# Kernel optimization log

Measured on AMD Instinct MI355X. Metric: run time of the kernel, lower is better.

## Reference

```python
import jax, jax.numpy as jnp
import numpy as np

B, S, D, W, P = 32, 512, 768, 256, 1024


def setup_inputs() -> dict:
    key = jax.random.key(0)
    k_h, k_len, k_pair, k_w1, k_w2 = jax.random.split(key, 5)
    h = jax.random.normal(k_h, (B, S, D), dtype=jnp.float32)
    # ragged word spans: each word covers 1 or 2 contiguous subwords; total <= S
    word_len = jax.random.randint(k_len, (B, W), 1, 3, dtype=jnp.int32)  # in {1,2}
    word_start = jnp.concatenate(
        [jnp.zeros((B, 1), jnp.int32), jnp.cumsum(word_len, axis=1)[:, :-1]], axis=1
    )
    # word-index pairs per configuration; -1 means "use zero embedding"
    pair_idx = jax.random.randint(k_pair, (B, P, 2), 0, W + 1, dtype=jnp.int32) - 1
    w1 = jax.random.normal(k_w1, (2 * D, 300), dtype=jnp.float32) * 0.02
    b1 = jnp.zeros((300,), jnp.float32)
    w2 = jax.random.normal(k_w2, (300, 4), dtype=jnp.float32) * 0.02
    b2 = jnp.zeros((4,), jnp.float32)
    return {"h": h, "w1": w1, "b1": b1, "w2": w2, "b2": b2,
            "word_start": word_start, "word_len": word_len, "pair_idx": pair_idx}


def reference(h, w1, b1, w2, b2, word_start, word_len, pair_idx):
    # --- mean-pool subword embeddings per word via prefix sums (segment mean) ---
    csum = jnp.cumsum(h, axis=1)                                   # [B,S,D]
    csum = jnp.concatenate([jnp.zeros_like(csum[:, :1]), csum], 1)  # [B,S+1,D]
    end = word_start + word_len                                     # [B,W]
    seg_sum = (jnp.take_along_axis(csum, end[:, :, None], axis=1)
               - jnp.take_along_axis(csum, word_start[:, :, None], axis=1))
    word_emb = seg_sum / word_len[:, :, None].astype(h.dtype)       # [B,W,D]
    # --- per-pair gather with -1 -> zero vector ---
    valid = (pair_idx >= 0)                                         # [B,P,2]
    idx = jnp.maximum(pair_idx, 0).reshape(h.shape[0], -1)          # [B,2P]
    emb = jnp.take_along_axis(word_emb, idx[:, :, None], axis=1)    # [B,2P,D]
    emb = emb.reshape(pair_idx.shape[0], pair_idx.shape[1], 2, -1)
    emb = jnp.where(valid[..., None], emb, jnp.zeros((), h.dtype))
    mlp_input = emb.reshape(-1, 2 * h.shape[-1])                    # [B*P, 2D]
    # --- tiny MLP + softmax (dropout is identity in eval) ---
    x = jnp.tanh(mlp_input @ w1 + b1)
    return jax.nn.softmax(x @ w2 + b2, axis=-1)                     # [B*P, 4]
```

## Files before the change

### kernel.cpp

```cpp
#include <hip/hip_runtime.h>
#include <cstddef>
#include <cstdint>

#define Bb   32
#define Ss   512
#define Dd   768
#define Ww   256
#define Pp   1024
#define NH   300
#define SLOT1 320
#define NPAD 640
#define Mm   (Bb * Ww)

typedef __attribute__((ext_vector_type(8))) short bf16x8;
typedef __attribute__((ext_vector_type(4))) float f32x4;

#define GPTR(p) ((const __attribute__((address_space(1))) void*)(p))
#define LPTR(p) ((__attribute__((address_space(3))) void*)(p))

__device__ __forceinline__ unsigned short f2bf(float x) {
    unsigned u = __builtin_bit_cast(unsigned, x);
    u += 0x7fffu + ((u >> 16) & 1u);
    return (unsigned short)(u >> 16);
}
__device__ __forceinline__ float bf2f(unsigned short u) {
    return __builtin_bit_cast(float, (unsigned)u << 16);
}
__device__ __forceinline__ float fast_tanh(float x) {
    x = fminf(fmaxf(x, -15.0f), 15.0f);
    float e = __expf(2.0f * x);
    return 1.0f - 2.0f * __builtin_amdgcn_rcpf(e + 1.0f);
}

__global__ __launch_bounds__(192) void prep_kernel(
    const float* __restrict__ h, const float* __restrict__ w1,
    const int* __restrict__ word_start, const int* __restrict__ word_len,
    unsigned short* __restrict__ emb, unsigned short* __restrict__ bmatT,
    unsigned short* __restrict__ zrow)
{
    const int bid = blockIdx.x;
    const int t   = threadIdx.x;
    if (bid < Mm) {
        const int m   = bid;
        const int b   = m >> 8;
        const int s0  = word_start[m];
        const int len = word_len[m];
        const float* p = h + (size_t)b * (Ss * Dd) + (size_t)s0 * Dd + t * 4;
        float4 v = *(const float4*)p;
        if (len == 2) {
            float4 v2 = *(const float4*)(p + Dd);
            v.x = (v.x + v2.x) * 0.5f;
            v.y = (v.y + v2.y) * 0.5f;
            v.z = (v.z + v2.z) * 0.5f;
            v.w = (v.w + v2.w) * 0.5f;
        }
        ushort4 o = make_ushort4(f2bf(v.x), f2bf(v.y), f2bf(v.z), f2bf(v.w));
        *(ushort4*)(emb + (size_t)m * Dd + t * 4) = o;
    } else if (bid < Mm + 4 * NPAD) {
        const int rb = bid - Mm;
        const int n  = rb >> 2;
        const int k  = ((rb & 3) * 192) + t;
        float v = 0.0f;
        if (n < NH)                          v = w1[(size_t)k * NH + n];
        else if (n >= SLOT1 && n < SLOT1+NH) v = w1[(size_t)(Dd + k) * NH + (n - SLOT1)];
        bmatT[(size_t)n * Dd + k] = f2bf(v);
    } else {
        if (t < NPAD / 4)
            *(ushort4*)(zrow + t * 4) = make_ushort4(0, 0, 0, 0);
    }
}

__global__ __launch_bounds__(256) void gemm_kernel(
    const unsigned short* __restrict__ emb, const unsigned short* __restrict__ bmatT,
    unsigned short* __restrict__ proj)
{
    __shared__ bf16x8 Al[2][4][128];
    __shared__ bf16x8 Bl[2][4][128];

    const int bid = blockIdx.x;
    const int t   = threadIdx.x;

    const int swz   = (bid & 7) * 40 + (bid >> 3);
    const int mBase = (swz / 5) * 128;
    const int nBase = (swz % 5) * 128;

    const int srow = t & 127;
    const int skb  = t >> 7;
    const unsigned short* srcA = emb   + (size_t)(mBase + srow) * Dd + (skb << 3);
    const unsigned short* srcB = bmatT + (size_t)(nBase + srow) * Dd + (skb << 3);
    char* ldsA = (char*)&Al[0][0][0] + t * 16;
    char* ldsB = (char*)&Bl[0][0][0] + t * 16;

    const int lane = t & 63;
    const int w    = t >> 6;
    const int wr   = w >> 1;
    const int wc   = w & 1;
    const int fr   = lane & 15;
    const int kb   = lane >> 4;

    f32x4 acc[4][4];
#pragma unroll
    for (int i = 0; i < 4; ++i)
#pragma unroll
        for (int j = 0; j < 4; ++j)
#pragma unroll
            for (int r = 0; r < 4; ++r) acc[i][j][r] = 0.0f;

#define STAGE(c, off)                                                                          \
    __builtin_amdgcn_global_load_lds(GPTR(srcA + (off)),      LPTR(ldsA + (c) * 8192),        16, 0, 0); \
    __builtin_amdgcn_global_load_lds(GPTR(srcA + (off) + 16), LPTR(ldsA + (c) * 8192 + 4096), 16, 0, 0); \
    __builtin_amdgcn_global_load_lds(GPTR(srcB + (off)),      LPTR(ldsB + (c) * 8192),        16, 0, 0); \
    __builtin_amdgcn_global_load_lds(GPTR(srcB + (off) + 16), LPTR(ldsB + (c) * 8192 + 4096), 16, 0, 0)

#define COMPUTE(c)                                                                             \
    {                                                                                          \
        bf16x8 a[4], b[4];                                                                     \
        _Pragma("unroll")                                                                      \
        for (int mi = 0; mi < 4; ++mi) a[mi] = Al[c][kb][wr * 64 + mi * 16 + fr];              \
        _Pragma("unroll")                                                                      \
        for (int ni = 0; ni < 4; ++ni) b[ni] = Bl[c][kb][wc * 64 + ni * 16 + fr];              \
        _Pragma("unroll")                                                                      \
        for (int mi = 0; mi < 4; ++mi)                                                         \
            _Pragma("unroll")                                                                  \
            for (int ni = 0; ni < 4; ++ni)                                                     \
                acc[mi][ni] = __builtin_amdgcn_mfma_f32_16x16x32_bf16(a[mi], b[ni], acc[mi][ni], 0, 0, 0); \
    }

    STAGE(0, 0);
    __syncthreads();
    int cur = 0;
    for (int k0 = 32; k0 < Dd; k0 += 32) {
        STAGE(cur ^ 1, k0);
        COMPUTE(cur);
        __syncthreads();
        cur ^= 1;
    }
    COMPUTE(cur);
#undef STAGE
#undef COMPUTE

    const int r0 = mBase + wr * 64 + kb * 4;
    const int c0 = nBase + wc * 64 + fr;
#pragma unroll
    for (int mi = 0; mi < 4; ++mi)
#pragma unroll
        for (int ni = 0; ni < 4; ++ni)
#pragma unroll
            for (int r = 0; r < 4; ++r)
                proj[(size_t)(r0 + mi * 16 + r) * NPAD + c0 + ni * 16] = f2bf(acc[mi][ni][r]);
}

__global__ __launch_bounds__(256) void mlp_kernel(
    const unsigned short* __restrict__ proj, const unsigned short* __restrict__ zrow,
    const float* __restrict__ b1, const float* __restrict__ w2,
    const float* __restrict__ b2, const int* __restrict__ pair_idx,
    float* __restrict__ out)
{
    const int wave = blockIdx.x * 4 + (threadIdx.x >> 6);
    const int lane = threadIdx.x & 63;
    const int wid0 = wave * 4;
    const int b    = wid0 >> 10;

    const int4 piA = *(const int4*)(pair_idx + wid0 * 2);
    const int4 piB = *(const int4*)(pair_idx + wid0 * 2 + 4);
    const int idx[8] = {piA.x, piA.y, piA.z, piA.w, piB.x, piB.y, piB.z, piB.w};

    const unsigned short* base = proj + (size_t)b * (Ww * NPAD);

    const unsigned short* r0p[4];
    const unsigned short* r1p[4];
#pragma unroll
    for (int p = 0; p < 4; ++p) {
        const int i0 = idx[p * 2], i1 = idx[p * 2 + 1];
        r0p[p] = (i0 >= 0) ? base + (size_t)i0 * NPAD : zrow;
        r1p[p] = ((i1 >= 0) ? base + (size_t)i1 * NPAD : zrow) + SLOT1;
    }

    unsigned short g0[4][5], g1[4][5];
#pragma unroll
    for (int p = 0; p < 4; ++p)
#pragma unroll
        for (int it = 0; it < 5; ++it) {
            const int j = lane + it * 64;
            g0[p][it] = r0p[p][j];
            g1[p][it] = r1p[p][j];
        }

    float acc[4][4];
#pragma unroll
    for (int p = 0; p < 4; ++p)
#pragma unroll
        for (int c = 0; c < 4; ++c) acc[p][c] = 0.0f;

#pragma unroll
    for (int it = 0; it < 5; ++it) {
        const int j  = lane + it * 64;
        const bool ok = (j < NH);
        const float bj = ok ? b1[j] : 0.0f;
        float4 wv = make_float4(0.f, 0.f, 0.f, 0.f);
        if (ok) wv = *(const float4*)(w2 + (size_t)j * 4);
#pragma unroll
        for (int p = 0; p < 4; ++p) {
            const float v = bj + bf2f(g0[p][it]) + bf2f(g1[p][it]);
            const float x = ok ? fast_tanh(v) : 0.0f;
            acc[p][0] = fmaf(x, wv.x, acc[p][0]);
            acc[p][1] = fmaf(x, wv.y, acc[p][1]);
            acc[p][2] = fmaf(x, wv.z, acc[p][2]);
            acc[p][3] = fmaf(x, wv.w, acc[p][3]);
        }
    }

#pragma unroll
    for (int off = 32; off >= 1; off >>= 1)
#pragma unroll
        for (int p = 0; p < 4; ++p)
#pragma unroll
            for (int c = 0; c < 4; ++c)
                acc[p][c] += __shfl_xor(acc[p][c], off, 64);

    float l0 = 0.f, l1 = 0.f, l2 = 0.f, l3 = 0.f;
#pragma unroll
    for (int p = 0; p < 4; ++p)
        if (lane == p) { l0 = acc[p][0]; l1 = acc[p][1]; l2 = acc[p][2]; l3 = acc[p][3]; }

    if (lane < 4) {
        l0 += b2[0]; l1 += b2[1]; l2 += b2[2]; l3 += b2[3];
        const float mx = fmaxf(fmaxf(l0, l1), fmaxf(l2, l3));
        const float e0 = __expf(l0 - mx), e1 = __expf(l1 - mx);
        const float e2 = __expf(l2 - mx), e3 = __expf(l3 - mx);
        const float inv = 1.0f / (e0 + e1 + e2 + e3);
        float4 o = {e0 * inv, e1 * inv, e2 * inv, e3 * inv};
        *(float4*)(out + (size_t)(wid0 + lane) * 4) = o;
    }
}

extern "C" void kernel_launch(void* const* d_in, const int* in_sizes, int n_in,
                              void* d_out, int out_size, void* d_ws, size_t ws_size,
                              hipStream_t stream)
{
    const float* h          = (const float*)d_in[0];
    const float* w1         = (const float*)d_in[1];
    const float* b1         = (const float*)d_in[2];
    const float* w2         = (const float*)d_in[3];
    const float* b2         = (const float*)d_in[4];
    const int*   word_start = (const int*)d_in[5];
    const int*   word_len   = (const int*)d_in[6];
    const int*   pair_idx   = (const int*)d_in[7];
    float*       out        = (float*)d_out;

    unsigned short* proj  = (unsigned short*)d_ws;
    unsigned short* emb   = (unsigned short*)((char*)d_ws + 10485760);
    unsigned short* bmatT = (unsigned short*)((char*)d_ws + 23068672);
    unsigned short* zrow  = (unsigned short*)((char*)d_ws + 24051712);

    prep_kernel<<<dim3(Mm + 4 * NPAD + 1), dim3(192), 0, stream>>>(
        h, w1, word_start, word_len, emb, bmatT, zrow);
    gemm_kernel<<<dim3(320), dim3(256), 0, stream>>>(emb, bmatT, proj);
    mlp_kernel <<<dim3(2048), dim3(256), 0, stream>>>(proj, zrow, b1, w2, b2, pair_idx, out);
}
```

Before: 53.59 us.

## Halve GEMM M-tile, process eight pairs per MLP wave, fold zero row into proj

The GEMM M-tile shrinks from 128 to 64 rows, so there are 640 blocks instead of 320 and the 256 CUs are filled more evenly. The MLP kernel now handles eight pairs per wave instead of four, gathering through integer offsets into proj, where the zero row now lives at the end of the buffer. This amortises the per-wave b1/w2 loads and the reduction overhead over more pairs. In exchange, each GEMM tile gets less data reuse, and the MLP wave holds more registers for eight pairs of gathered values, which may lower occupancy.

```diff
diff --git a/kernel.cpp b/kernel.cpp
--- a/kernel.cpp
+++ b/kernel.cpp
@@ -11,6 +11,7 @@
 #define SLOT1 320
 #define NPAD 640
 #define Mm   (Bb * Ww)
+#define ZOFF (Mm * NPAD)
 
 typedef __attribute__((ext_vector_type(8))) short bf16x8;
 typedef __attribute__((ext_vector_type(4))) float f32x4;
@@ -36,7 +37,7 @@
     const float* __restrict__ h, const float* __restrict__ w1,
     const int* __restrict__ word_start, const int* __restrict__ word_len,
     unsigned short* __restrict__ emb, unsigned short* __restrict__ bmatT,
-    unsigned short* __restrict__ zrow)
+    unsigned short* __restrict__ proj)
 {
     const int bid = blockIdx.x;
     const int t   = threadIdx.x;
@@ -61,12 +62,12 @@
         const int n  = rb >> 2;
         const int k  = ((rb & 3) * 192) + t;
         float v = 0.0f;
-        if (n < NH)                          v = w1[(size_t)k * NH + n];
-        else if (n >= SLOT1 && n < SLOT1+NH) v = w1[(size_t)(Dd + k) * NH + (n - SLOT1)];
+        if (n < NH)                            v = w1[(size_t)k * NH + n];
+        else if (n >= SLOT1 && n < SLOT1 + NH) v = w1[(size_t)(Dd + k) * NH + (n - SLOT1)];
         bmatT[(size_t)n * Dd + k] = f2bf(v);
     } else {
         if (t < NPAD / 4)
-            *(ushort4*)(zrow + t * 4) = make_ushort4(0, 0, 0, 0);
+            *(ushort4*)(proj + ZOFF + t * 4) = make_ushort4(0, 0, 0, 0);
     }
 }
 
@@ -74,20 +75,18 @@
     const unsigned short* __restrict__ emb, const unsigned short* __restrict__ bmatT,
     unsigned short* __restrict__ proj)
 {
-    __shared__ bf16x8 Al[2][4][128];
+    __shared__ bf16x8 Al[2][4][64];
     __shared__ bf16x8 Bl[2][4][128];
 
     const int bid = blockIdx.x;
     const int t   = threadIdx.x;
 
-    const int swz   = (bid & 7) * 40 + (bid >> 3);
-    const int mBase = (swz / 5) * 128;
+    const int swz   = (bid & 7) * 80 + (bid >> 3);
+    const int mBase = (swz / 5) * 64;
     const int nBase = (swz % 5) * 128;
 
-    const int srow = t & 127;
-    const int skb  = t >> 7;
-    const unsigned short* srcA = emb   + (size_t)(mBase + srow) * Dd + (skb << 3);
-    const unsigned short* srcB = bmatT + (size_t)(nBase + srow) * Dd + (skb << 3);
+    const unsigned short* srcA = emb   + (size_t)(mBase + (t & 63))  * Dd + ((t >> 6) << 3);
+    const unsigned short* srcB = bmatT + (size_t)(nBase + (t & 127)) * Dd + ((t >> 7) << 3);
     char* ldsA = (char*)&Al[0][0][0] + t * 16;
     char* ldsB = (char*)&Bl[0][0][0] + t * 16;
 
@@ -98,29 +97,28 @@
     const int fr   = lane & 15;
     const int kb   = lane >> 4;
 
-    f32x4 acc[4][4];
-#pragma unroll
-    for (int i = 0; i < 4; ++i)
+    f32x4 acc[2][4];
+#pragma unroll
+    for (int i = 0; i < 2; ++i)
 #pragma unroll
         for (int j = 0; j < 4; ++j)
 #pragma unroll
             for (int r = 0; r < 4; ++r) acc[i][j][r] = 0.0f;
 
 #define STAGE(c, off)                                                                          \
-    __builtin_amdgcn_global_load_lds(GPTR(srcA + (off)),      LPTR(ldsA + (c) * 8192),        16, 0, 0); \
-    __builtin_amdgcn_global_load_lds(GPTR(srcA + (off) + 16), LPTR(ldsA + (c) * 8192 + 4096), 16, 0, 0); \
+    __builtin_amdgcn_global_load_lds(GPTR(srcA + (off)),      LPTR(ldsA + (c) * 4096),        16, 0, 0); \
     __builtin_amdgcn_global_load_lds(GPTR(srcB + (off)),      LPTR(ldsB + (c) * 8192),        16, 0, 0); \
     __builtin_amdgcn_global_load_lds(GPTR(srcB + (off) + 16), LPTR(ldsB + (c) * 8192 + 4096), 16, 0, 0)
 
 #define COMPUTE(c)                                                                             \
     {                                                                                          \
-        bf16x8 a[4], b[4];                                                                     \
+        bf16x8 a[2], b[4];                                                                     \
         _Pragma("unroll")                                                                      \
-        for (int mi = 0; mi < 4; ++mi) a[mi] = Al[c][kb][wr * 64 + mi * 16 + fr];              \
+        for (int mi = 0; mi < 2; ++mi) a[mi] = Al[c][kb][wr * 32 + mi * 16 + fr];              \
         _Pragma("unroll")                                                                      \
         for (int ni = 0; ni < 4; ++ni) b[ni] = Bl[c][kb][wc * 64 + ni * 16 + fr];              \
         _Pragma("unroll")                                                                      \
-        for (int mi = 0; mi < 4; ++mi)                                                         \
+        for (int mi = 0; mi < 2; ++mi)                                                         \
             _Pragma("unroll")                                                                  \
             for (int ni = 0; ni < 4; ++ni)                                                     \
                 acc[mi][ni] = __builtin_amdgcn_mfma_f32_16x16x32_bf16(a[mi], b[ni], acc[mi][ni], 0, 0, 0); \
@@ -139,10 +137,10 @@
 #undef STAGE
 #undef COMPUTE
 
-    const int r0 = mBase + wr * 64 + kb * 4;
+    const int r0 = mBase + wr * 32 + kb * 4;
     const int c0 = nBase + wc * 64 + fr;
 #pragma unroll
-    for (int mi = 0; mi < 4; ++mi)
+    for (int mi = 0; mi < 2; ++mi)
 #pragma unroll
         for (int ni = 0; ni < 4; ++ni)
 #pragma unroll
@@ -151,44 +149,46 @@
 }
 
 __global__ __launch_bounds__(256) void mlp_kernel(
-    const unsigned short* __restrict__ proj, const unsigned short* __restrict__ zrow,
+    const unsigned short* __restrict__ proj,
     const float* __restrict__ b1, const float* __restrict__ w2,
     const float* __restrict__ b2, const int* __restrict__ pair_idx,
     float* __restrict__ out)
 {
     const int wave = blockIdx.x * 4 + (threadIdx.x >> 6);
     const int lane = threadIdx.x & 63;
-    const int wid0 = wave * 4;
+    const int wid0 = wave * 8;
     const int b    = wid0 >> 10;
-
-    const int4 piA = *(const int4*)(pair_idx + wid0 * 2);
-    const int4 piB = *(const int4*)(pair_idx + wid0 * 2 + 4);
-    const int idx[8] = {piA.x, piA.y, piA.z, piA.w, piB.x, piB.y, piB.z, piB.w};
-
-    const unsigned short* base = proj + (size_t)b * (Ww * NPAD);
-
-    const unsigned short* r0p[4];
-    const unsigned short* r1p[4];
-#pragma unroll
-    for (int p = 0; p < 4; ++p) {
+    const int wbase = b * Ww;
+
+    int idx[16];
+#pragma unroll
+    for (int q = 0; q < 4; ++q) {
+        const int4 pi = *(const int4*)(pair_idx + wid0 * 2 + q * 4);
+        idx[q * 4 + 0] = pi.x; idx[q * 4 + 1] = pi.y;
+        idx[q * 4 + 2] = pi.z; idx[q * 4 + 3] = pi.w;
+    }
+
+    int off0[8], off1[8];
+#pragma unroll
+    for (int p = 0; p < 8; ++p) {
         const int i0 = idx[p * 2], i1 = idx[p * 2 + 1];
-        r0p[p] = (i0 >= 0) ? base + (size_t)i0 * NPAD : zrow;
-        r1p[p] = ((i1 >= 0) ? base + (size_t)i1 * NPAD : zrow) + SLOT1;
-    }
-
-    unsigned short g0[4][5], g1[4][5];
-#pragma unroll
-    for (int p = 0; p < 4; ++p)
+        off0[p] = (i0 >= 0) ? (wbase + i0) * NPAD : ZOFF;
+        off1[p] = ((i1 >= 0) ? (wbase + i1) * NPAD : ZOFF) + SLOT1;
+    }
+
+    unsigned short g0[8][5], g1[8][5];
+#pragma unroll
+    for (int p = 0; p < 8; ++p)
 #pragma unroll
         for (int it = 0; it < 5; ++it) {
             const int j = lane + it * 64;
-            g0[p][it] = r0p[p][j];
-            g1[p][it] = r1p[p][j];
+            g0[p][it] = proj[(size_t)off0[p] + j];
+            g1[p][it] = proj[(size_t)off1[p] + j];
         }
 
-    float acc[4][4];
-#pragma unroll
-    for (int p = 0; p < 4; ++p)
+    float acc[8][4];
+#pragma unroll
+    for (int p = 0; p < 8; ++p)
 #pragma unroll
         for (int c = 0; c < 4; ++c) acc[p][c] = 0.0f;
 
@@ -200,7 +200,7 @@
         float4 wv = make_float4(0.f, 0.f, 0.f, 0.f);
         if (ok) wv = *(const float4*)(w2 + (size_t)j * 4);
 #pragma unroll
-        for (int p = 0; p < 4; ++p) {
+        for (int p = 0; p < 8; ++p) {
             const float v = bj + bf2f(g0[p][it]) + bf2f(g1[p][it]);
             const float x = ok ? fast_tanh(v) : 0.0f;
             acc[p][0] = fmaf(x, wv.x, acc[p][0]);
@@ -213,17 +213,17 @@
 #pragma unroll
     for (int off = 32; off >= 1; off >>= 1)
 #pragma unroll
-        for (int p = 0; p < 4; ++p)
+        for (int p = 0; p < 8; ++p)
 #pragma unroll
             for (int c = 0; c < 4; ++c)
                 acc[p][c] += __shfl_xor(acc[p][c], off, 64);
 
     float l0 = 0.f, l1 = 0.f, l2 = 0.f, l3 = 0.f;
 #pragma unroll
-    for (int p = 0; p < 4; ++p)
+    for (int p = 0; p < 8; ++p)
         if (lane == p) { l0 = acc[p][0]; l1 = acc[p][1]; l2 = acc[p][2]; l3 = acc[p][3]; }
 
-    if (lane < 4) {
+    if (lane < 8) {
         l0 += b2[0]; l1 += b2[1]; l2 += b2[2]; l3 += b2[3];
         const float mx = fmaxf(fmaxf(l0, l1), fmaxf(l2, l3));
         const float e0 = __expf(l0 - mx), e1 = __expf(l1 - mx);
@@ -249,12 +249,11 @@
     float*       out        = (float*)d_out;
 
     unsigned short* proj  = (unsigned short*)d_ws;
-    unsigned short* emb   = (unsigned short*)((char*)d_ws + 10485760);
-    unsigned short* bmatT = (unsigned short*)((char*)d_ws + 23068672);
-    unsigned short* zrow  = (unsigned short*)((char*)d_ws + 24051712);
+    unsigned short* emb   = (unsigned short*)((char*)d_ws + 16777216);
+    unsigned short* bmatT = (unsigned short*)((char*)d_ws + 31457280);
 
     prep_kernel<<<dim3(Mm + 4 * NPAD + 1), dim3(192), 0, stream>>>(
-        h, w1, word_start, word_len, emb, bmatT, zrow);
-    gemm_kernel<<<dim3(320), dim3(256), 0, stream>>>(emb, bmatT, proj);
-    mlp_kernel <<<dim3(2048), dim3(256), 0, stream>>>(proj, zrow, b1, w2, b2, pair_idx, out);
-}
+        h, w1, word_start, word_len, emb, bmatT, proj);
+    gemm_kernel<<<dim3(640), dim3(256), 0, stream>>>(emb, bmatT, proj);
+    mlp_kernel <<<dim3(1024), dim3(256), 0, stream>>>(proj, b1, w2, b2, pair_idx, out);
+}
```

Measured after the change: 58.09 us. 1.08x slower.

## Use grid-stride prep kernel and LDS-transpose reduction in MLP epilogue

Applied to the files above, without the earlier changes.

The prep kernel goes from one block per word row (over 10k small blocks) to a fixed 1024-block grid-stride loop over flat element indices. The w1 transpose/pack loop now walks n fastest, so reads of w1 are coalesced but writes to bmatT become strided. The MLP kernel replaces the 6-step, 16-value butterfly shuffle reduction with an LDS transpose: each lane sums 16 entries, then a few shuffles finish the reduction and a lane-parallel softmax follows. This adds shared memory and a block barrier, and a division by 192 per element in prep.

```diff
diff --git a/kernel.cpp b/kernel.cpp
--- a/kernel.cpp
+++ b/kernel.cpp
@@ -32,20 +32,22 @@
     return 1.0f - 2.0f * __builtin_amdgcn_rcpf(e + 1.0f);
 }
 
-__global__ __launch_bounds__(192) void prep_kernel(
+__global__ __launch_bounds__(256) void prep_kernel(
     const float* __restrict__ h, const float* __restrict__ w1,
     const int* __restrict__ word_start, const int* __restrict__ word_len,
     unsigned short* __restrict__ emb, unsigned short* __restrict__ bmatT,
     unsigned short* __restrict__ zrow)
 {
-    const int bid = blockIdx.x;
-    const int t   = threadIdx.x;
-    if (bid < Mm) {
-        const int m   = bid;
+    const int gid    = blockIdx.x * 256 + threadIdx.x;
+    const int stride = 1024 * 256;
+
+    for (int u = gid; u < Mm * 192; u += stride) {
+        const int m = u / 192;
+        const int c = u - m * 192;
         const int b   = m >> 8;
         const int s0  = word_start[m];
         const int len = word_len[m];
-        const float* p = h + (size_t)b * (Ss * Dd) + (size_t)s0 * Dd + t * 4;
+        const float* p = h + (size_t)b * (Ss * Dd) + (size_t)s0 * Dd + c * 4;
         float4 v = *(const float4*)p;
         if (len == 2) {
             float4 v2 = *(const float4*)(p + Dd);
@@ -55,19 +57,20 @@
             v.w = (v.w + v2.w) * 0.5f;
         }
         ushort4 o = make_ushort4(f2bf(v.x), f2bf(v.y), f2bf(v.z), f2bf(v.w));
-        *(ushort4*)(emb + (size_t)m * Dd + t * 4) = o;
-    } else if (bid < Mm + 4 * NPAD) {
-        const int rb = bid - Mm;
-        const int n  = rb >> 2;
-        const int k  = ((rb & 3) * 192) + t;
+        *(ushort4*)(emb + (size_t)m * Dd + c * 4) = o;
+    }
+
+    for (int u = gid; u < Dd * NPAD; u += stride) {
+        const int k = u / NPAD;
+        const int n = u - k * NPAD;
         float v = 0.0f;
-        if (n < NH)                          v = w1[(size_t)k * NH + n];
-        else if (n >= SLOT1 && n < SLOT1+NH) v = w1[(size_t)(Dd + k) * NH + (n - SLOT1)];
+        if (n < NH)                            v = w1[(size_t)k * NH + n];
+        else if (n >= SLOT1 && n < SLOT1 + NH) v = w1[(size_t)(Dd + k) * NH + (n - SLOT1)];
         bmatT[(size_t)n * Dd + k] = f2bf(v);
-    } else {
-        if (t < NPAD / 4)
-            *(ushort4*)(zrow + t * 4) = make_ushort4(0, 0, 0, 0);
-    }
+    }
+
+    if (gid < NPAD / 4)
+        *(ushort4*)(zrow + gid * 4) = make_ushort4(0, 0, 0, 0);
 }
 
 __global__ __launch_bounds__(256) void gemm_kernel(
@@ -156,16 +159,18 @@
     const float* __restrict__ b2, const int* __restrict__ pair_idx,
     float* __restrict__ out)
 {
-    const int wave = blockIdx.x * 4 + (threadIdx.x >> 6);
+    __shared__ float red[4][64][17];
+
+    const int wv   = threadIdx.x >> 6;
+    const int wave = blockIdx.x * 4 + wv;
     const int lane = threadIdx.x & 63;
     const int wid0 = wave * 4;
     const int b    = wid0 >> 10;
+    const unsigned short* base = proj + (size_t)b * (Ww * NPAD);
 
     const int4 piA = *(const int4*)(pair_idx + wid0 * 2);
     const int4 piB = *(const int4*)(pair_idx + wid0 * 2 + 4);
     const int idx[8] = {piA.x, piA.y, piA.z, piA.w, piB.x, piB.y, piB.z, piB.w};
-
-    const unsigned short* base = proj + (size_t)b * (Ww * NPAD);
 
     const unsigned short* r0p[4];
     const unsigned short* r1p[4];
@@ -197,41 +202,45 @@
         const int j  = lane + it * 64;
         const bool ok = (j < NH);
         const float bj = ok ? b1[j] : 0.0f;
-        float4 wv = make_float4(0.f, 0.f, 0.f, 0.f);
-        if (ok) wv = *(const float4*)(w2 + (size_t)j * 4);
+        float4 wv4 = make_float4(0.f, 0.f, 0.f, 0.f);
+        if (ok) wv4 = *(const float4*)(w2 + (size_t)j * 4);
 #pragma unroll
         for (int p = 0; p < 4; ++p) {
             const float v = bj + bf2f(g0[p][it]) + bf2f(g1[p][it]);
             const float x = ok ? fast_tanh(v) : 0.0f;
-            acc[p][0] = fmaf(x, wv.x, acc[p][0]);
-            acc[p][1] = fmaf(x, wv.y, acc[p][1]);
-            acc[p][2] = fmaf(x, wv.z, acc[p][2]);
-            acc[p][3] = fmaf(x, wv.w, acc[p][3]);
+            acc[p][0] = fmaf(x, wv4.x, acc[p][0]);
+            acc[p][1] = fmaf(x, wv4.y, acc[p][1]);
+            acc[p][2] = fmaf(x, wv4.z, acc[p][2]);
+            acc[p][3] = fmaf(x, wv4.w, acc[p][3]);
         }
     }
 
 #pragma unroll
-    for (int off = 32; off >= 1; off >>= 1)
-#pragma unroll
-        for (int p = 0; p < 4; ++p)
-#pragma unroll
-            for (int c = 0; c < 4; ++c)
-                acc[p][c] += __shfl_xor(acc[p][c], off, 64);
-
-    float l0 = 0.f, l1 = 0.f, l2 = 0.f, l3 = 0.f;
-#pragma unroll
     for (int p = 0; p < 4; ++p)
-        if (lane == p) { l0 = acc[p][0]; l1 = acc[p][1]; l2 = acc[p][2]; l3 = acc[p][3]; }
-
-    if (lane < 4) {
-        l0 += b2[0]; l1 += b2[1]; l2 += b2[2]; l3 += b2[3];
-        const float mx = fmaxf(fmaxf(l0, l1), fmaxf(l2, l3));
-        const float e0 = __expf(l0 - mx), e1 = __expf(l1 - mx);
-        const float e2 = __expf(l2 - mx), e3 = __expf(l3 - mx);
-        const float inv = 1.0f / (e0 + e1 + e2 + e3);
-        float4 o = {e0 * inv, e1 * inv, e2 * inv, e3 * inv};
-        *(float4*)(out + (size_t)(wid0 + lane) * 4) = o;
-    }
+#pragma unroll
+        for (int c = 0; c < 4; ++c)
+            red[wv][lane][p * 4 + c] = acc[p][c];
+    __syncthreads();
+
+    const int o = lane >> 2;
+    const int g = lane & 3;
+    float v = 0.0f;
+#pragma unroll
+    for (int i = 0; i < 16; ++i)
+        v += red[wv][g * 16 + i][o];
+    v += __shfl_xor(v, 1, 64);
+    v += __shfl_xor(v, 2, 64);
+
+    const int c = o & 3;
+    const float l = v + b2[c];
+    float mx = fmaxf(l, __shfl_xor(l, 4, 64));
+    mx = fmaxf(mx, __shfl_xor(mx, 8, 64));
+    const float e = __expf(l - mx);
+    float s = e + __shfl_xor(e, 4, 64);
+    s += __shfl_xor(s, 8, 64);
+    const float r = e * __builtin_amdgcn_rcpf(s);
+    if (g == 0)
+        out[(size_t)(wid0 + (o >> 2)) * 4 + c] = r;
 }
 
 extern "C" void kernel_launch(void* const* d_in, const int* in_sizes, int n_in,
@@ -253,7 +262,7 @@
     unsigned short* bmatT = (unsigned short*)((char*)d_ws + 23068672);
     unsigned short* zrow  = (unsigned short*)((char*)d_ws + 24051712);
 
-    prep_kernel<<<dim3(Mm + 4 * NPAD + 1), dim3(192), 0, stream>>>(
+    prep_kernel<<<dim3(1024), dim3(256), 0, stream>>>(
         h, w1, word_start, word_len, emb, bmatT, zrow);
     gemm_kernel<<<dim3(320), dim3(256), 0, stream>>>(emb, bmatT, proj);
     mlp_kernel <<<dim3(2048), dim3(256), 0, stream>>>(proj, zrow, b1, w2, b2, pair_idx, out);
```

Measured after the change: 52.16 us. 2.7% less time.
